# Kernel optimization log

Measured on AMD Instinct MI355X. Metric: run time of the kernel, lower is better.

## Reference

```python
import jax, jax.numpy as jnp
import numpy as np

HIDDEN, N_HEADS, HEAD_DIM, CACHE_LEN, BATCH = 4096, 32, 128, 512, 32


def setup_inputs() -> dict:
    key = jax.random.key(0)
    ks = jax.random.split(key, 7)
    s = 0.02
    return {
        "x": jax.random.normal(ks[0], (BATCH, 1, HIDDEN), jnp.float32),
        "k_cache": jax.random.normal(ks[1], (BATCH, N_HEADS, CACHE_LEN, HEAD_DIM), jnp.float32),
        "v_cache": jax.random.normal(ks[2], (BATCH, N_HEADS, CACHE_LEN, HEAD_DIM), jnp.float32),
        # torch nn.Linear weights: (out_features, in_features), y = x @ W.T
        "wq": jax.random.normal(ks[3], (N_HEADS * HEAD_DIM, HIDDEN), jnp.float32) * s,
        "wk": jax.random.normal(ks[4], (N_HEADS * HEAD_DIM, HIDDEN), jnp.float32) * s,
        "wv": jax.random.normal(ks[5], (N_HEADS * HEAD_DIM, HIDDEN), jnp.float32) * s,
        "wo": jax.random.normal(ks[6], (HIDDEN, N_HEADS * HEAD_DIM), jnp.float32) * s,
    }


def reference(x, k_cache, v_cache, wq, wk, wv, wo):
    bsz = x.shape[0]
    # projections: (b, 1, H*D) -> (b, n_heads, 1, head_dim)
    def proj(w):
        return (x @ w.T).reshape(bsz, 1, N_HEADS, HEAD_DIM).transpose(0, 2, 1, 3)
    q, k_new, v_new = proj(wq), proj(wk), proj(wv)
    scale = 1.0 / HEAD_DIM ** 0.5
    # cache attention: (b, h, 1, cache_len)
    cache_scores = jnp.einsum("bhqd,bhkd->bhqk", q, k_cache) * scale
    cache_probs = jax.nn.softmax(cache_scores, axis=-1)
    cache_out = jnp.einsum("bhqk,bhkd->bhqd", cache_probs, v_cache)
    # new-token attention: softmax over a single key (probs == 1), kept faithful
    new_scores = jnp.einsum("bhqd,bhkd->bhqk", q, k_new) * scale
    new_probs = jax.nn.softmax(new_scores, axis=-1)
    new_out = jnp.einsum("bhqk,bhkd->bhqd", new_probs, v_new)
    out = cache_out + new_out  # note: sum of two separately-normalized softmaxes (as in source)
    out = out.transpose(0, 2, 1, 3).reshape(bsz, 1, N_HEADS * HEAD_DIM)
    return out @ wo.T
```

## Files before the change

kernel.cpp:

```cpp
#include <hip/hip_runtime.h>
#include <hip/hip_bf16.h>

#define HIDDEN 4096
#define NHEADS 32
#define HDIM 128
#define CLEN 512
#define BATCH 32

__device__ __forceinline__ void proj_body(const float* __restrict__ X,
                                          const float* __restrict__ W,
                                          float* __restrict__ Y,
                                          int rowblock) {
    const int t   = threadIdx.x;
    const int l   = t & 63;
    const int wid = t >> 6;
    const int rowbase = rowblock * 8;
    const float* wp = W + (size_t)rowbase * HIDDEN + 4 * l;
    const float* xp = X + (size_t)(wid * 4) * HIDDEN + 4 * l;

    float v[32];
    #pragma unroll
    for (int j = 0; j < 32; ++j) v[j] = 0.f;

    #pragma unroll 2
    for (int kp = 0; kp < HIDDEN; kp += 256) {
        float4 wv[8], xv[4];
        #pragma unroll
        for (int r = 0; r < 8; ++r)
            wv[r] = *(const float4*)(wp + (size_t)r * HIDDEN + kp);
        #pragma unroll
        for (int b = 0; b < 4; ++b)
            xv[b] = *(const float4*)(xp + (size_t)b * HIDDEN + kp);
        #pragma unroll
        for (int r = 0; r < 8; ++r) {
            #pragma unroll
            for (int b = 0; b < 4; ++b) {
                v[r * 4 + b] += wv[r].x * xv[b].x + wv[r].y * xv[b].y +
                                wv[r].z * xv[b].z + wv[r].w * xv[b].w;
            }
        }
    }

    #pragma unroll
    for (int j = 0; j < 32; ++j) v[j] += __shfl_xor(v[j], 1);
    #pragma unroll
    for (int s = 1; s <= 5; ++s) {
        const int m = 1 << s;
        const int bit = (l >> s) & 1;
        #pragma unroll
        for (int i = 0; i < (32 >> s); ++i) {
            float t0 = __shfl_xor(v[2 * i], m);
            float t1 = __shfl_xor(v[2 * i + 1], m);
            v[i] = bit ? (v[2 * i + 1] + t1) : (v[2 * i] + t0);
        }
    }
    if (!(l & 1)) {
        const int j = l >> 1;
        const int r = j >> 2, b = j & 3;
        Y[(size_t)(wid * 4 + b) * HIDDEN + rowbase + r] = v[0];
    }
}

__global__ __launch_bounds__(512, 2) void proj_dual_kernel(const float* __restrict__ X,
                                                           const float* __restrict__ Wa,
                                                           const float* __restrict__ Wb,
                                                           float* __restrict__ Ya,
                                                           float* __restrict__ Yb) {
    const int bx = blockIdx.x;
    proj_body(X, (bx & 1) ? Wb : Wa, (bx & 1) ? Yb : Ya, bx >> 1);
}

__global__ __launch_bounds__(512, 2) void proj_out_kernel(const float* __restrict__ X,
                                                          const float* __restrict__ W,
                                                          float* __restrict__ Y) {
    proj_body(X, W, Y, blockIdx.x);
}

#define KB 256

__global__ __launch_bounds__(256, 8) void attn_split_kernel(
        const float* __restrict__ q,
        const float* __restrict__ kc,
        const float* __restrict__ vc,
        float* __restrict__ o_half,
        float* __restrict__ ms,
        float* __restrict__ ss) {
    __shared__ float sc[KB];
    __shared__ float red[8];
    __shared__ float part[4 * HDIM];
    const int t = threadIdx.x;
    const int w = t >> 6;
    const int l = t & 63;
    const int bid = blockIdx.x;
    const int bh = bid >> 1;
    const int half = bid & 1;
    const int b = bh >> 5, h = bh & 31;
    const int kbase = half * KB;
    const float* K = kc + (size_t)bh * CLEN * HDIM + (size_t)kbase * HDIM;
    const float* V = vc + (size_t)bh * CLEN * HDIM + (size_t)kbase * HDIM;
    const float scale = 0.088388347648318447f;
    const int d0 = 4 * (l & 31);
    const int kh = l >> 5;
    float4 q4 = *(const float4*)(q + (size_t)b * HIDDEN + h * HDIM + d0);

    const int kw = w * 64;
    #pragma unroll 8
    for (int r = 0; r < 32; ++r) {
        const int k = kw + 2 * r + kh;
        float4 kv = *(const float4*)(K + (size_t)k * HDIM + d0);
        float p = q4.x * kv.x + q4.y * kv.y + q4.z * kv.z + q4.w * kv.w;
        #pragma unroll
        for (int m = 16; m; m >>= 1) p += __shfl_xor(p, m);
        if ((l & 31) == 0) sc[k] = p * scale;
    }
    __syncthreads();

    float s = sc[t];
    float mx = s;
    #pragma unroll
    for (int m = 32; m; m >>= 1) mx = fmaxf(mx, __shfl_xor(mx, m));
    if (l == 0) red[w] = mx;
    __syncthreads();
    mx = fmaxf(fmaxf(red[0], red[1]), fmaxf(red[2], red[3]));
    float e = __expf(s - mx);
    sc[t] = e;
    float es = e;
    #pragma unroll
    for (int m = 32; m; m >>= 1) es += __shfl_xor(es, m);
    if (l == 0) red[4 + w] = es;
    __syncthreads();
    if (t == 0) {
        ms[bid] = mx;
        ss[bid] = red[4] + red[5] + red[6] + red[7];
    }

    float4 acc = make_float4(0.f, 0.f, 0.f, 0.f);
    #pragma unroll 8
    for (int k = kw; k < kw + 64; k += 2) {
        float4 v4 = *(const float4*)(V + (size_t)(k + kh) * HDIM + d0);
        float p = sc[k + kh];
        acc.x += p * v4.x; acc.y += p * v4.y;
        acc.z += p * v4.z; acc.w += p * v4.w;
    }
    acc.x += __shfl_xor(acc.x, 32);
    acc.y += __shfl_xor(acc.y, 32);
    acc.z += __shfl_xor(acc.z, 32);
    acc.w += __shfl_xor(acc.w, 32);
    if (l < 32) *(float4*)(&part[w * HDIM + d0]) = acc;
    __syncthreads();
    if (t < HDIM) {
        float r = part[t] + part[HDIM + t] + part[2 * HDIM + t] + part[3 * HDIM + t];
        o_half[(size_t)bid * HDIM + t] = r;
    }
}

__global__ __launch_bounds__(256) void combine_kernel(
        const float* __restrict__ o_half,
        const float* __restrict__ ms,
        const float* __restrict__ ss,
        const float* __restrict__ vnew,
        float* __restrict__ attn_out) {
    const int t = threadIdx.x;
    const int bh = blockIdx.x * 2 + (t >> 7);
    const int d = t & 127;
    const float m0 = ms[2 * bh], m1 = ms[2 * bh + 1];
    const float s0 = ss[2 * bh], s1 = ss[2 * bh + 1];
    const float M = fmaxf(m0, m1);
    const float w0 = __expf(m0 - M), w1 = __expf(m1 - M);
    const float inv = 1.0f / (s0 * w0 + s1 * w1);
    const float o0 = o_half[(size_t)(2 * bh) * HDIM + d];
    const float o1 = o_half[(size_t)(2 * bh + 1) * HDIM + d];
    const int b = bh >> 5, h = bh & 31;
    const size_t idx = (size_t)b * HIDDEN + h * HDIM + d;
    attn_out[idx] = (o0 * w0 + o1 * w1) * inv + vnew[idx];
}

extern "C" void kernel_launch(void* const* d_in, const int* in_sizes, int n_in,
                              void* d_out, int out_size, void* d_ws, size_t ws_size,
                              hipStream_t stream) {
    (void)in_sizes; (void)n_in; (void)out_size; (void)ws_size;
    const float* x  = (const float*)d_in[0];
    const float* kc = (const float*)d_in[1];
    const float* vc = (const float*)d_in[2];
    const float* wq = (const float*)d_in[3];
    const float* wv = (const float*)d_in[5];
    const float* wo = (const float*)d_in[6];
    float* out = (float*)d_out;

    float* q      = (float*)d_ws;
    float* vnew   = q + BATCH * HIDDEN;
    float* attn   = vnew + BATCH * HIDDEN;
    float* o_half = attn + BATCH * HIDDEN;
    float* ms     = o_half + 2 * BATCH * NHEADS * HDIM;
    float* ss     = ms + 2 * BATCH * NHEADS;

    proj_dual_kernel<<<2 * (HIDDEN / 8), 512, 0, stream>>>(x, wq, wv, q, vnew);
    attn_split_kernel<<<2 * BATCH * NHEADS, 256, 0, stream>>>(q, kc, vc, o_half, ms, ss);
    combine_kernel<<<BATCH * NHEADS / 2, 256, 0, stream>>>(o_half, ms, ss, vnew, attn);
    proj_out_kernel<<<HIDDEN / 8, 512, 0, stream>>>(attn, wo, out);
}
```

Baseline: 198.7 us.

## Overlap V projection with cache attention in one interleaved kernel launch

The Q and V projections are split apart. Only Q is computed first, by a new 256-thread projection body that handles 4 weight rows by 8 batch rows. The V projection blocks are interleaved (one in every three blocks) with the cache-attention blocks in a single launch, so the weight-bandwidth-bound projection overlaps the KV-cache streaming. The attention loads also switch to nontemporal loads, and each block starts at a rotated key offset, which likely aims to spread accesses across memory channels. The risks are imbalance between the two kinds of block in the mixed kernel and a different projection tiling for Q.

```diff
diff --git a/kernel.cpp b/kernel.cpp
--- a/kernel.cpp
+++ b/kernel.cpp
@@ -6,6 +6,9 @@
 #define HDIM 128
 #define CLEN 512
 #define BATCH 32
+#define KB 256
+
+typedef float f32x4 __attribute__((ext_vector_type(4)));
 
 __device__ __forceinline__ void proj_body(const float* __restrict__ X,
                                           const float* __restrict__ W,
@@ -61,53 +64,101 @@
     }
 }
 
-__global__ __launch_bounds__(512, 2) void proj_dual_kernel(const float* __restrict__ X,
-                                                           const float* __restrict__ Wa,
-                                                           const float* __restrict__ Wb,
-                                                           float* __restrict__ Ya,
-                                                           float* __restrict__ Yb) {
-    const int bx = blockIdx.x;
-    proj_body(X, (bx & 1) ? Wb : Wa, (bx & 1) ? Yb : Ya, bx >> 1);
-}
-
 __global__ __launch_bounds__(512, 2) void proj_out_kernel(const float* __restrict__ X,
                                                           const float* __restrict__ W,
                                                           float* __restrict__ Y) {
     proj_body(X, W, Y, blockIdx.x);
 }
 
-#define KB 256
-
-__global__ __launch_bounds__(256, 8) void attn_split_kernel(
-        const float* __restrict__ q,
-        const float* __restrict__ kc,
-        const float* __restrict__ vc,
-        float* __restrict__ o_half,
-        float* __restrict__ ms,
-        float* __restrict__ ss) {
+__device__ __forceinline__ void proj4_body(const float* __restrict__ X,
+                                           const float* __restrict__ W,
+                                           float* __restrict__ Y,
+                                           int rowblock) {
+    const int t   = threadIdx.x;
+    const int l   = t & 63;
+    const int wid = t >> 6;
+    const int rowbase = rowblock * 4;
+    const float* wp = W + (size_t)rowbase * HIDDEN + 4 * l;
+    const float* xp = X + (size_t)(wid * 8) * HIDDEN + 4 * l;
+
+    float v[32];
+    #pragma unroll
+    for (int j = 0; j < 32; ++j) v[j] = 0.f;
+
+    #pragma unroll 2
+    for (int kp = 0; kp < HIDDEN; kp += 256) {
+        float4 wv[4], xv[8];
+        #pragma unroll
+        for (int r = 0; r < 4; ++r)
+            wv[r] = *(const float4*)(wp + (size_t)r * HIDDEN + kp);
+        #pragma unroll
+        for (int b = 0; b < 8; ++b)
+            xv[b] = *(const float4*)(xp + (size_t)b * HIDDEN + kp);
+        #pragma unroll
+        for (int r = 0; r < 4; ++r) {
+            #pragma unroll
+            for (int b = 0; b < 8; ++b) {
+                v[r * 8 + b] += wv[r].x * xv[b].x + wv[r].y * xv[b].y +
+                                wv[r].z * xv[b].z + wv[r].w * xv[b].w;
+            }
+        }
+    }
+
+    #pragma unroll
+    for (int j = 0; j < 32; ++j) v[j] += __shfl_xor(v[j], 1);
+    #pragma unroll
+    for (int s = 1; s <= 5; ++s) {
+        const int m = 1 << s;
+        const int bit = (l >> s) & 1;
+        #pragma unroll
+        for (int i = 0; i < (32 >> s); ++i) {
+            float t0 = __shfl_xor(v[2 * i], m);
+            float t1 = __shfl_xor(v[2 * i + 1], m);
+            v[i] = bit ? (v[2 * i + 1] + t1) : (v[2 * i] + t0);
+        }
+    }
+    if (!(l & 1)) {
+        const int j = l >> 1;
+        const int r = j >> 3, b = j & 7;
+        Y[(size_t)(wid * 8 + b) * HIDDEN + rowbase + r] = v[0];
+    }
+}
+
+__global__ __launch_bounds__(256) void proj_q_kernel(const float* __restrict__ X,
+                                                     const float* __restrict__ W,
+                                                     float* __restrict__ Y) {
+    proj4_body(X, W, Y, blockIdx.x);
+}
+
+__device__ __forceinline__ void attn_body(const float* __restrict__ q,
+                                          const float* __restrict__ kc,
+                                          const float* __restrict__ vc,
+                                          float* __restrict__ o_half,
+                                          float* __restrict__ ms,
+                                          float* __restrict__ ss,
+                                          int bid) {
     __shared__ float sc[KB];
     __shared__ float red[8];
     __shared__ float part[4 * HDIM];
     const int t = threadIdx.x;
     const int w = t >> 6;
     const int l = t & 63;
-    const int bid = blockIdx.x;
     const int bh = bid >> 1;
     const int half = bid & 1;
     const int b = bh >> 5, h = bh & 31;
-    const int kbase = half * KB;
-    const float* K = kc + (size_t)bh * CLEN * HDIM + (size_t)kbase * HDIM;
-    const float* V = vc + (size_t)bh * CLEN * HDIM + (size_t)kbase * HDIM;
+    const float* K = kc + (size_t)bh * CLEN * HDIM + (size_t)(half * KB) * HDIM;
+    const float* V = vc + (size_t)bh * CLEN * HDIM + (size_t)(half * KB) * HDIM;
     const float scale = 0.088388347648318447f;
     const int d0 = 4 * (l & 31);
     const int kh = l >> 5;
+    const int start = ((bid * 37) & 127) * 2;
     float4 q4 = *(const float4*)(q + (size_t)b * HIDDEN + h * HDIM + d0);
 
     const int kw = w * 64;
     #pragma unroll 8
     for (int r = 0; r < 32; ++r) {
-        const int k = kw + 2 * r + kh;
-        float4 kv = *(const float4*)(K + (size_t)k * HDIM + d0);
+        const int k = (((kw + 2 * r) + start) & (KB - 1)) + kh;
+        f32x4 kv = __builtin_nontemporal_load((const f32x4*)(K + (size_t)k * HDIM + d0));
         float p = q4.x * kv.x + q4.y * kv.y + q4.z * kv.z + q4.w * kv.w;
         #pragma unroll
         for (int m = 16; m; m >>= 1) p += __shfl_xor(p, m);
@@ -136,9 +187,10 @@
 
     float4 acc = make_float4(0.f, 0.f, 0.f, 0.f);
     #pragma unroll 8
-    for (int k = kw; k < kw + 64; k += 2) {
-        float4 v4 = *(const float4*)(V + (size_t)(k + kh) * HDIM + d0);
-        float p = sc[k + kh];
+    for (int kk = 0; kk < 64; kk += 2) {
+        const int k = (((kw + kk) + start) & (KB - 1)) + kh;
+        f32x4 v4 = __builtin_nontemporal_load((const f32x4*)(V + (size_t)k * HDIM + d0));
+        float p = sc[k];
         acc.x += p * v4.x; acc.y += p * v4.y;
         acc.z += p * v4.z; acc.w += p * v4.w;
     }
@@ -152,6 +204,21 @@
         float r = part[t] + part[HDIM + t] + part[2 * HDIM + t] + part[3 * HDIM + t];
         o_half[(size_t)bid * HDIM + t] = r;
     }
+}
+
+__global__ __launch_bounds__(256) void attn_projv_kernel(
+        const float* __restrict__ q, const float* __restrict__ kc,
+        const float* __restrict__ vc, const float* __restrict__ x,
+        const float* __restrict__ wv_m, float* __restrict__ vnew,
+        float* __restrict__ o_half, float* __restrict__ ms,
+        float* __restrict__ ss) {
+    const int bid = blockIdx.x;
+    const int sel = bid % 3;
+    if (sel == 2) {
+        proj4_body(x, wv_m, vnew, bid / 3);
+        return;
+    }
+    attn_body(q, kc, vc, o_half, ms, ss, (bid / 3) * 2 + sel);
 }
 
 __global__ __launch_bounds__(256) void combine_kernel(
@@ -194,8 +261,9 @@
     float* ms     = o_half + 2 * BATCH * NHEADS * HDIM;
     float* ss     = ms + 2 * BATCH * NHEADS;
 
-    proj_dual_kernel<<<2 * (HIDDEN / 8), 512, 0, stream>>>(x, wq, wv, q, vnew);
-    attn_split_kernel<<<2 * BATCH * NHEADS, 256, 0, stream>>>(q, kc, vc, o_half, ms, ss);
+    proj_q_kernel<<<HIDDEN / 4, 256, 0, stream>>>(x, wq, q);
+    attn_projv_kernel<<<3072, 256, 0, stream>>>(q, kc, vc, x, wv, vnew,
+                                                o_half, ms, ss);
     combine_kernel<<<BATCH * NHEADS / 2, 256, 0, stream>>>(o_half, ms, ss, vnew, attn);
     proj_out_kernel<<<HIDDEN / 8, 512, 0, stream>>>(attn, wo, out);
 }
```

Result: faster. 185.9 us (-6.5%).
